# Kernel tuning notes

Measured on AMD Instinct MI355X. Metric: run time of the kernel, lower is better.

Reference implementation:

```python
import jax, jax.numpy as jnp
import numpy as np

N = 65536        # total nodes (32 graphs x 2048 nodes)
E = 1048576      # total edges (avg degree 16)
D = 64           # in_dim
H = 64           # hidden_dim
O = 32           # out_dim
B = 32           # number of graphs in the batch
NPG = 2048       # nodes per graph
EPS = 1e-5
SLOPE = 0.01     # LeakyReLU negative slope


def setup_inputs() -> dict:
    key = jax.random.key(0)
    ks = jax.random.split(key, 7)
    x = jax.random.normal(ks[0], (N, D), jnp.float32)
    edge_weights = jax.random.uniform(ks[1], (E,), jnp.float32)
    src = jax.random.randint(ks[2], (E,), 0, N, dtype=jnp.int32)
    dst = jax.random.randint(ks[3], (E,), 0, N, dtype=jnp.int32)
    graph_ids = (jnp.arange(N, dtype=jnp.int32) // NPG).astype(jnp.int32)
    # DGL GraphConv weight is (in_feats, out_feats); Linear weight is (out, in)
    W1 = jax.random.normal(ks[4], (D, H), jnp.float32) * np.float32(1.0 / np.sqrt(D))
    W2 = jax.random.normal(ks[5], (H, H), jnp.float32) * np.float32(1.0 / np.sqrt(H))
    Wc = jax.random.normal(ks[6], (O, H), jnp.float32) * np.float32(1.0 / np.sqrt(H))
    gn1_w = jnp.ones((H,), jnp.float32); gn1_b = jnp.zeros((H,), jnp.float32); gn1_a = jnp.ones((H,), jnp.float32)
    gn2_w = jnp.ones((H,), jnp.float32); gn2_b = jnp.zeros((H,), jnp.float32); gn2_a = jnp.ones((H,), jnp.float32)
    return dict(x=x, edge_weights=edge_weights, W1=W1, W2=W2, Wc=Wc,
                gn1_w=gn1_w, gn1_b=gn1_b, gn1_a=gn1_a,
                gn2_w=gn2_w, gn2_b=gn2_b, gn2_a=gn2_a,
                src=src, dst=dst, graph_ids=graph_ids)


def _graph_conv(h, W, src, dst, ew, inv_sqrt_out, inv_sqrt_in):
    # DGL GraphConv norm='both' with edge_weight:
    # out = D_in^{-1/2} * scatter_sum( ew * (D_out^{-1/2} h W)[src] -> dst )
    h = (h * inv_sqrt_out[:, None]) @ W                       # [N,H]
    m = h[src] * ew[:, None]                                  # [E,H] gather + edge weight
    agg = jax.ops.segment_sum(m, dst, num_segments=N)         # [N,H] scatter
    return agg * inv_sqrt_in[:, None]


def _graph_norm(x, w, b, a):
    # GraphNorm: (x - a*mean) / sqrt(var(x - a*mean) + eps) * w + b, stats over node dim
    mean = jnp.mean(x, axis=0, keepdims=True)
    sub = x - a * mean
    std = jnp.sqrt(jnp.mean(sub * sub, axis=0, keepdims=True) + EPS)
    return w * (sub / std) + b


def _leaky(x):
    return jnp.where(x >= 0, x, SLOPE * x)


def reference(x, edge_weights, W1, W2, Wc,
              gn1_w, gn1_b, gn1_a, gn2_w, gn2_b, gn2_a,
              src, dst, graph_ids):
    ones_e = jnp.ones((E,), x.dtype)
    deg_out = jnp.maximum(jax.ops.segment_sum(ones_e, src, num_segments=N), 1.0)
    deg_in = jnp.maximum(jax.ops.segment_sum(ones_e, dst, num_segments=N), 1.0)
    inv_so = jax.lax.rsqrt(deg_out)
    inv_si = jax.lax.rsqrt(deg_in)

    h = _graph_conv(x, W1, src, dst, edge_weights, inv_so, inv_si)
    h = _graph_norm(_leaky(h), gn1_w, gn1_b, gn1_a)
    h = _graph_conv(h, W2, src, dst, edge_weights, inv_so, inv_si)
    h = _graph_norm(_leaky(h), gn2_w, gn2_b, gn2_a)

    # dgl.mean_nodes: per-graph mean pooling
    counts = jax.ops.segment_sum(jnp.ones((N,), x.dtype), graph_ids, num_segments=B)
    pooled = jax.ops.segment_sum(h, graph_ids, num_segments=B) / counts[:, None]  # [B,H]
    return pooled @ Wc.T  # [B,O]
```

## Files before the change

kernel.cpp:

```cpp
#include <hip/hip_runtime.h>

#define N_NODES 65536
#define N_EDGES 1048576
#define B_GRAPHS 32
#define NPG     2048
#define EPS_GN  1e-5f
#define SLOPE   0.01f
#define NBUCKET 256
#define STRIDE_B 4608
#define ECAP    1024

typedef unsigned short ushort_t;
typedef unsigned int uint_t;

static __device__ __forceinline__ ushort_t f2bf(float f) {
    uint_t u = __float_as_uint(f);
    return (ushort_t)((u + 0x7FFFu + ((u >> 16) & 1u)) >> 16);
}

static __device__ __forceinline__ void acc_bf8(float4& a0, float4& a1, uint4 u, float w) {
    a0.x += __uint_as_float(u.x << 16) * w;
    a0.y += __uint_as_float(u.x & 0xffff0000u) * w;
    a0.z += __uint_as_float(u.y << 16) * w;
    a0.w += __uint_as_float(u.y & 0xffff0000u) * w;
    a1.x += __uint_as_float(u.z << 16) * w;
    a1.y += __uint_as_float(u.z & 0xffff0000u) * w;
    a1.z += __uint_as_float(u.w << 16) * w;
    a1.w += __uint_as_float(u.w & 0xffff0000u) * w;
}

__global__ __launch_bounds__(256) void hist_kernel(const int4* __restrict__ src4,
                                                   unsigned int* __restrict__ partial,
                                                   int* __restrict__ cursor) {
    __shared__ unsigned int bins[16384];
    int tid = threadIdx.x, c = blockIdx.x;
#pragma unroll
    for (int k = 0; k < 64; ++k) bins[k * 256 + tid] = 0u;
    if (c == 0) cursor[tid] = tid * STRIDE_B;
    __syncthreads();
#pragma unroll
    for (int k = 0; k < 8; ++k) {
        int4 v = src4[c * 2048 + k * 256 + tid];
        atomicAdd(&bins[v.x >> 2], 1u << ((v.x & 3) * 8));
        atomicAdd(&bins[v.y >> 2], 1u << ((v.y & 3) * 8));
        atomicAdd(&bins[v.z >> 2], 1u << ((v.z & 3) * 8));
        atomicAdd(&bins[v.w >> 2], 1u << ((v.w & 3) * 8));
    }
    __syncthreads();
    unsigned int* dstp = partial + c * 16384;
#pragma unroll
    for (int k = 0; k < 64; ++k) dstp[k * 256 + tid] = bins[k * 256 + tid];
}

__global__ __launch_bounds__(256) void reduce_src(const unsigned int* __restrict__ partial,
                                                  float4* __restrict__ inv_so4) {
    int w = blockIdx.x * 256 + threadIdx.x;
    unsigned int s0 = 0, s1 = 0, s2 = 0, s3 = 0;
#pragma unroll
    for (int c = 0; c < 128; ++c) {
        unsigned int v = partial[c * 16384 + w];
        s0 += v & 255u; s1 += (v >> 8) & 255u; s2 += (v >> 16) & 255u; s3 += v >> 24;
    }
    float4 r;
    r.x = rsqrtf((float)max((int)s0, 1));
    r.y = rsqrtf((float)max((int)s1, 1));
    r.z = rsqrtf((float)max((int)s2, 1));
    r.w = rsqrtf((float)max((int)s3, 1));
    inv_so4[w] = r;
}

__global__ __launch_bounds__(256) void bucket_scatter(const int4* __restrict__ src4,
                                                      const int4* __restrict__ dst4,
                                                      const float4* __restrict__ ew4,
                                                      int* __restrict__ cursor,
                                                      int2* __restrict__ bedges) {
    __shared__ int lhist[NBUCKET];
    __shared__ int lstart[NBUCKET];
    __shared__ int gbase[NBUCKET];
    __shared__ int sc[NBUCKET];
    __shared__ int2 staged[2048];
    int tid = threadIdx.x;
    int vbase = blockIdx.x * 512;
    lhist[tid] = 0;
    __syncthreads();
    int w0[8]; int wbr[8]; float wwt[8];
#pragma unroll
    for (int k = 0; k < 2; ++k) {
        int4 s = src4[vbase + k * 256 + tid];
        int4 d = dst4[vbase + k * 256 + tid];
        float4 w = ew4[vbase + k * 256 + tid];
        int ss[4] = {s.x, s.y, s.z, s.w};
        int dd[4] = {d.x, d.y, d.z, d.w};
        float wf[4] = {w.x, w.y, w.z, w.w};
#pragma unroll
        for (int j = 0; j < 4; ++j) {
            int b = dd[j] >> 8;
            w0[k * 4 + j] = ss[j] | ((dd[j] & 255) << 16);
            wwt[k * 4 + j] = wf[j];
            int r = atomicAdd(&lhist[b], 1);
            wbr[k * 4 + j] = (b << 16) | r;
        }
    }
    __syncthreads();
    int cnt = lhist[tid];
    sc[tid] = cnt;
    __syncthreads();
    for (int off = 1; off < 256; off <<= 1) {
        int t = (tid >= off) ? sc[tid - off] : 0;
        __syncthreads();
        sc[tid] += t;
        __syncthreads();
    }
    lstart[tid] = sc[tid] - cnt;
    gbase[tid] = cnt ? atomicAdd(&cursor[tid], cnt) : 0;
    __syncthreads();
#pragma unroll
    for (int k = 0; k < 8; ++k)
        staged[lstart[wbr[k] >> 16] + (wbr[k] & 0xFFFF)] =
            make_int2(w0[k], __float_as_int(wwt[k]));
    __syncthreads();
    int gb = gbase[tid], ls = lstart[tid];
    for (int i = 0; i < cnt; ++i)
        bedges[gb + i] = staged[ls + i];
}

__global__ __launch_bounds__(1024) void refine_kernel(const int2* __restrict__ bedges,
                                                      const int* __restrict__ cursor,
                                                      int* __restrict__ rowp,
                                                      int* __restrict__ deg,
                                                      float* __restrict__ inv_si,
                                                      int2* __restrict__ csr) {
    __shared__ int hist[4096];
    __shared__ int sc[256];
    __shared__ int2 staged[STRIDE_B];
    int tid = threadIdx.x, b = blockIdx.x;
    int e0 = b * STRIDE_B;
    int nE = cursor[b] - e0;
    for (int k = tid; k < 4096; k += 1024) hist[k] = 0;
    __syncthreads();
    for (int i = tid; i < nE; i += 1024) {
        int2 e = bedges[e0 + i];
        staged[i] = e;
        int key = (((e.x >> 16) & 255) << 4) | ((e.x & 0xFFFF) >> 12);
        atomicAdd(&hist[key], 1);
    }
    __syncthreads();
    int loc[16];
    int run = 0;
    if (tid < 256) {
        int base = tid << 4;
#pragma unroll
        for (int j = 0; j < 16; ++j) { loc[j] = run; run += hist[base + j]; }
        sc[tid] = run;
    }
    __syncthreads();
    for (int off = 1; off < 256; off <<= 1) {
        int t = (tid >= off && tid < 256) ? sc[tid - off] : 0;
        __syncthreads();
        if (tid < 256) sc[tid] += t;
        __syncthreads();
    }
    if (tid < 256) {
        int start = sc[tid] - run;
        rowp[b * 256 + tid] = e0 + start;
        deg[b * 256 + tid] = run;
        inv_si[b * 256 + tid] = rsqrtf((float)max(run, 1));
        int base = tid << 4;
#pragma unroll
        for (int j = 0; j < 16; ++j) hist[base + j] = start + loc[j];
    }
    __syncthreads();
    for (int i = tid; i < nE; i += 1024) {
        int2 e = staged[i];
        int key = (((e.x >> 16) & 255) << 4) | ((e.x & 0xFFFF) >> 12);
        int pos = atomicAdd(&hist[key], 1);
        csr[e0 + pos] = make_int2(e.x & 0xFFFF, e.y);
    }
}

__global__ __launch_bounds__(256) void gemm_f32(const float* __restrict__ in,
                                                const float* __restrict__ W,
                                                const float* __restrict__ inv_so,
                                                ushort_t* __restrict__ out_bf) {
    __shared__ float wT[64][68];
    __shared__ float xlds[16][64];
    int tid = threadIdx.x;
#pragma unroll
    for (int j = 0; j < 16; ++j) {
        int i = j * 256 + tid;
        wT[i & 63][i >> 6] = W[i];
    }
    int r0 = blockIdx.x * 16;
#pragma unroll
    for (int j = 0; j < 4; ++j) {
        int i = j * 256 + tid;
        int r = i >> 6, k = i & 63;
        int gr = r0 + r;
        xlds[r][k] = in[(size_t)gr * 64 + k] * inv_so[gr];
    }
    __syncthreads();
    int c = tid & 63;
    int rg = tid >> 6;
    float acc[4] = {0.f, 0.f, 0.f, 0.f};
#pragma unroll
    for (int k0 = 0; k0 < 64; k0 += 4) {
        float4 wv = *(const float4*)&wT[c][k0];
#pragma unroll
        for (int j = 0; j < 4; ++j) {
            float4 xv = *(const float4*)&xlds[rg * 4 + j][k0];
            acc[j] += xv.x * wv.x + xv.y * wv.y + xv.z * wv.z + xv.w * wv.w;
        }
    }
#pragma unroll
    for (int j = 0; j < 4; ++j)
        out_bf[(size_t)(r0 + rg * 4 + j) * 64 + c] = f2bf(acc[j]);
}

__global__ __launch_bounds__(256) void gemm_bf16(const ushort_t* __restrict__ in,
                                                 const float* __restrict__ W,
                                                 const float* __restrict__ inv_so,
                                                 const float* __restrict__ alpha,
                                                 const float* __restrict__ beta,
                                                 ushort_t* __restrict__ out_bf) {
    __shared__ float wT[64][68];
    __shared__ float xlds[16][64];
    int tid = threadIdx.x;
#pragma unroll
    for (int j = 0; j < 16; ++j) {
        int i = j * 256 + tid;
        wT[i & 63][i >> 6] = W[i];
    }
    int r0 = blockIdx.x * 16;
    const uint_t* inU = (const uint_t*)in;
#pragma unroll
    for (int j = 0; j < 2; ++j) {
        int idx = j * 256 + tid;
        int r = idx >> 5, kp = idx & 31;
        int gr = r0 + r;
        uint_t u = inU[(size_t)gr * 32 + kp];
        int k0 = kp * 2;
        float lo = __uint_as_float(u << 16);
        float hi = __uint_as_float(u & 0xffff0000u);
        float iso = inv_so[gr];
        xlds[r][k0]     = (alpha[k0] * lo + beta[k0]) * iso;
        xlds[r][k0 + 1] = (alpha[k0 + 1] * hi + beta[k0 + 1]) * iso;
    }
    __syncthreads();
    int c = tid & 63;
    int rg = tid >> 6;
    float acc[4] = {0.f, 0.f, 0.f, 0.f};
#pragma unroll
    for (int k0 = 0; k0 < 64; k0 += 4) {
        float4 wv = *(const float4*)&wT[c][k0];
#pragma unroll
        for (int j = 0; j < 4; ++j) {
            float4 xv = *(const float4*)&xlds[rg * 4 + j][k0];
            acc[j] += xv.x * wv.x + xv.y * wv.y + xv.z * wv.z + xv.w * wv.w;
        }
    }
#pragma unroll
    for (int j = 0; j < 4; ++j)
        out_bf[(size_t)(r0 + rg * 4 + j) * 64 + c] = f2bf(acc[j]);
}

__global__ __launch_bounds__(256) void agg_kernel(const ushort_t* __restrict__ Tb,
                                                  const int* __restrict__ rowp,
                                                  const int* __restrict__ deg,
                                                  const float* __restrict__ inv_si,
                                                  const int2* __restrict__ csr,
                                                  ushort_t* __restrict__ Yb,
                                                  float4* __restrict__ statsP4) {
    __shared__ long est[ECAP];
    int tid = threadIdx.x;
    int slot = tid >> 3;
    int node0 = blockIdx.x * 32;
    int node = node0 + slot;
    int l8 = tid & 7;
    int e_start = rowp[node0];
    int e_end = rowp[node0 + 31] + deg[node0 + 31];
    int nE = e_end - e_start;
    const long* gedge = (const long*)(csr + e_start);
    for (int i = tid; i < nE && i < ECAP; i += 256)
        est[i] = gedge[i];
    __syncthreads();
    int off = rowp[node] - e_start;
    int cnt = deg[node];
    int m1 = min(cnt, max(0, ECAP - off));
    float4 a0 = make_float4(0.f, 0.f, 0.f, 0.f);
    float4 a1 = make_float4(0.f, 0.f, 0.f, 0.f);
    int i = 0;
    for (; i + 8 <= m1; i += 8) {
        long e[8];
#pragma unroll
        for (int k = 0; k < 8; ++k) e[k] = est[off + i + k];
        uint4 t[8];
#pragma unroll
        for (int k = 0; k < 8; ++k)
            t[k] = ((const uint4*)(Tb + (((size_t)(e[k] & 0xFFFF)) << 6)))[l8];
#pragma unroll
        for (int k = 0; k < 8; ++k)
            acc_bf8(a0, a1, t[k], __int_as_float((int)(e[k] >> 32)));
    }
    for (; i < m1; ++i) {
        long e = est[off + i];
        uint4 u = ((const uint4*)(Tb + (((size_t)(e & 0xFFFF)) << 6)))[l8];
        acc_bf8(a0, a1, u, __int_as_float((int)(e >> 32)));
    }
    for (; i < cnt; ++i) {
        long e = gedge[off + i];
        uint4 u = ((const uint4*)(Tb + (((size_t)(e & 0xFFFF)) << 6)))[l8];
        acc_bf8(a0, a1, u, __int_as_float((int)(e >> 32)));
    }
    float s = inv_si[node];
    float4 v0, v1;
    v0.x = a0.x * s; v0.x = (v0.x >= 0.f) ? v0.x : SLOPE * v0.x;
    v0.y = a0.y * s; v0.y = (v0.y >= 0.f) ? v0.y : SLOPE * v0.y;
    v0.z = a0.z * s; v0.z = (v0.z >= 0.f) ? v0.z : SLOPE * v0.z;
    v0.w = a0.w * s; v0.w = (v0.w >= 0.f) ? v0.w : SLOPE * v0.w;
    v1.x = a1.x * s; v1.x = (v1.x >= 0.f) ? v1.x : SLOPE * v1.x;
    v1.y = a1.y * s; v1.y = (v1.y >= 0.f) ? v1.y : SLOPE * v1.y;
    v1.z = a1.z * s; v1.z = (v1.z >= 0.f) ? v1.z : SLOPE * v1.z;
    v1.w = a1.w * s; v1.w = (v1.w >= 0.f) ? v1.w : SLOPE * v1.w;
    if (Yb) {
        uint_t p0 = (uint_t)f2bf(v0.x) | ((uint_t)f2bf(v0.y) << 16);
        uint_t p1 = (uint_t)f2bf(v0.z) | ((uint_t)f2bf(v0.w) << 16);
        uint_t p2 = (uint_t)f2bf(v1.x) | ((uint_t)f2bf(v1.y) << 16);
        uint_t p3 = (uint_t)f2bf(v1.z) | ((uint_t)f2bf(v1.w) << 16);
        ((uint4*)Yb)[(size_t)node * 8 + l8] = make_uint4(p0, p1, p2, p3);
    }
    float4 s0 = v0, s1 = v1;
    float4 q0 = make_float4(v0.x * v0.x, v0.y * v0.y, v0.z * v0.z, v0.w * v0.w);
    float4 q1 = make_float4(v1.x * v1.x, v1.y * v1.y, v1.z * v1.z, v1.w * v1.w);
#pragma unroll
    for (int m = 8; m <= 32; m <<= 1) {
        s0.x += __shfl_xor(s0.x, m); s0.y += __shfl_xor(s0.y, m);
        s0.z += __shfl_xor(s0.z, m); s0.w += __shfl_xor(s0.w, m);
        s1.x += __shfl_xor(s1.x, m); s1.y += __shfl_xor(s1.y, m);
        s1.z += __shfl_xor(s1.z, m); s1.w += __shfl_xor(s1.w, m);
        q0.x += __shfl_xor(q0.x, m); q0.y += __shfl_xor(q0.y, m);
        q0.z += __shfl_xor(q0.z, m); q0.w += __shfl_xor(q0.w, m);
        q1.x += __shfl_xor(q1.x, m); q1.y += __shfl_xor(q1.y, m);
        q1.z += __shfl_xor(q1.z, m); q1.w += __shfl_xor(q1.w, m);
    }
    int ln = tid & 63;
    if (ln < 8) {
        float4* row = statsP4 + ((size_t)blockIdx.x * 4 + (tid >> 6)) * 32;
        row[ln * 2 + 0] = s0;
        row[ln * 2 + 1] = s1;
        row[16 + ln * 2 + 0] = q0;
        row[16 + ln * 2 + 1] = q1;
    }
}

__global__ __launch_bounds__(256) void reduce_statsA(const float* __restrict__ statsP,
                                                     float* __restrict__ slab) {
    __shared__ float red[256];
    int tid = threadIdx.x, b = blockIdx.x;
    int col = tid & 127, half = tid >> 7;
    float s = 0.f;
    for (int i = half; i < 128; i += 2)
        s += statsP[(size_t)(b * 128 + i) * 128 + col];
    red[tid] = s;
    __syncthreads();
    if (tid < 128) slab[b * 128 + tid] = red[tid] + red[tid + 128];
}

__global__ __launch_bounds__(256) void reduce_stats2(const float* __restrict__ statsP,
                                                     float* __restrict__ slab,
                                                     float* __restrict__ pooledSum) {
    __shared__ float red[256];
    int tid = threadIdx.x, b = blockIdx.x;
    if (b < 64) {
        int col = tid & 127, half = tid >> 7;
        float s = 0.f;
        for (int i = half; i < 128; i += 2)
            s += statsP[(size_t)(b * 128 + i) * 128 + col];
        red[tid] = s;
        __syncthreads();
        if (tid < 128) slab[b * 128 + tid] = red[tid] + red[tid + 128];
    } else {
        int g = b - 64;
        int col = tid & 63, part = tid >> 6;
        float s = 0.f;
        for (int r = g * 256 + part; r < (g + 1) * 256; r += 4)
            s += statsP[(size_t)r * 128 + col];
        red[tid] = s;
        __syncthreads();
        if (tid < 64)
            pooledSum[g * 64 + tid] =
                red[tid] + red[tid + 64] + red[tid + 128] + red[tid + 192];
    }
}

__global__ void finalize_kernel(const float* __restrict__ slab,
                                const float* __restrict__ w, const float* __restrict__ b,
                                const float* __restrict__ a,
                                float* __restrict__ alpha, float* __restrict__ beta) {
    int f = threadIdx.x;
    float Sy = 0.f, Qy = 0.f;
    for (int i = 0; i < 64; ++i) {
        Sy += slab[i * 128 + f];
        Qy += slab[i * 128 + 64 + f];
    }
    float m = Sy * (1.f / N_NODES);
    float q = Qy * (1.f / N_NODES);
    float af = a[f];
    float var = q - 2.f * af * m * m + af * af * m * m;
    float al = w[f] / sqrtf(var + EPS_GN);
    alpha[f] = al;
    beta[f] = b[f] - al * af * m;
}

__global__ __launch_bounds__(256) void out_kernel(const float* __restrict__ slab2,
                                                  const float* __restrict__ gn_w,
                                                  const float* __restrict__ gn_b,
                                                  const float* __restrict__ gn_a,
                                                  const float* __restrict__ pooledSum,
                                                  const float* __restrict__ Wc,
                                                  float* __restrict__ out) {
    __shared__ float al[64], be[64];
    __shared__ float p[B_GRAPHS * 64];
    int tid = threadIdx.x;
    if (tid < 64) {
        float Sy = 0.f, Qy = 0.f;
        for (int i = 0; i < 64; ++i) {
            Sy += slab2[i * 128 + tid];
            Qy += slab2[i * 128 + 64 + tid];
        }
        float m = Sy * (1.f / N_NODES);
        float q = Qy * (1.f / N_NODES);
        float af = gn_a[tid];
        float var = q - 2.f * af * m * m + af * af * m * m;
        float a_ = gn_w[tid] / sqrtf(var + EPS_GN);
        al[tid] = a_;
        be[tid] = gn_b[tid] - a_ * af * m;
    }
    __syncthreads();
    for (int i = tid; i < B_GRAPHS * 64; i += 256) {
        int f = i & 63;
        p[i] = al[f] * (pooledSum[i] * (1.f / NPG)) + be[f];
    }
    __syncthreads();
    for (int idx = tid; idx < B_GRAPHS * 32; idx += 256) {
        int g = idx >> 5, o = idx & 31;
        float acc = 0.f;
        for (int f = 0; f < 64; ++f)
            acc += p[g * 64 + f] * Wc[o * 64 + f];
        out[idx] = acc;
    }
}

extern "C" void kernel_launch(void* const* d_in, const int* in_sizes, int n_in,
                              void* d_out, int out_size, void* d_ws, size_t ws_size,
                              hipStream_t stream) {
    const float* x     = (const float*)d_in[0];
    const float* ew    = (const float*)d_in[1];
    const float* W1    = (const float*)d_in[2];
    const float* W2    = (const float*)d_in[3];
    const float* Wc    = (const float*)d_in[4];
    const float* gn1_w = (const float*)d_in[5];
    const float* gn1_b = (const float*)d_in[6];
    const float* gn1_a = (const float*)d_in[7];
    const float* gn2_w = (const float*)d_in[8];
    const float* gn2_b = (const float*)d_in[9];
    const float* gn2_a = (const float*)d_in[10];
    const int* src     = (const int*)d_in[11];
    const int* dst     = (const int*)d_in[12];

    char* ws = (char*)d_ws;
    int*   cursor    = (int*)(ws + 0);
    float* ab1       = (float*)(ws + 4096);
    float* pooledSum = (float*)(ws + 8192);
    float* slab1     = (float*)(ws + 16384);
    float* slab2     = (float*)(ws + 49152);
    int*   rowp      = (int*)(ws + 131072);
    int*   deg       = (int*)(ws + 393216);
    float* inv_so    = (float*)(ws + 655360);
    float* inv_si    = (float*)(ws + 917504);
    unsigned int* partial = (unsigned int*)(ws + (2u << 20));
    int2*  bedges    = (int2*)(ws + (10u << 20));
    int2*  csr       = (int2*)(ws + (20u << 20));
    ushort_t* Tbf    = (ushort_t*)(ws + (30u << 20));
    ushort_t* Ybf    = (ushort_t*)(ws + (38u << 20));
    float* statsP    = (float*)(ws + (46u << 20));

    hist_kernel<<<128, 256, 0, stream>>>((const int4*)src, partial, cursor);
    reduce_src<<<64, 256, 0, stream>>>(partial, (float4*)inv_so);
    bucket_scatter<<<512, 256, 0, stream>>>((const int4*)src, (const int4*)dst,
                                            (const float4*)ew, cursor, bedges);
    refine_kernel<<<NBUCKET, 1024, 0, stream>>>(bedges, cursor, rowp, deg, inv_si, csr);

    gemm_f32<<<N_NODES / 16, 256, 0, stream>>>(x, W1, inv_so, Tbf);
    agg_kernel<<<N_NODES / 32, 256, 0, stream>>>(Tbf, rowp, deg, inv_si, csr,
                                                 Ybf, (float4*)statsP);
    reduce_statsA<<<64, 256, 0, stream>>>(statsP, slab1);
    finalize_kernel<<<1, 64, 0, stream>>>(slab1, gn1_w, gn1_b, gn1_a, ab1 + 0, ab1 + 64);

    gemm_bf16<<<N_NODES / 16, 256, 0, stream>>>(Ybf, W2, inv_so, ab1 + 0, ab1 + 64, Tbf);
    agg_kernel<<<N_NODES / 32, 256, 0, stream>>>(Tbf, rowp, deg, inv_si, csr,
                                                 nullptr, (float4*)statsP);
    reduce_stats2<<<96, 256, 0, stream>>>(statsP, slab2, pooledSum);

    out_kernel<<<1, 256, 0, stream>>>(slab2, gn2_w, gn2_b, gn2_a, pooledSum, Wc,
                                      (float*)d_out);
}
```

Measured before the change: 172.5 us.

## Fuse per-bucket CSR refine into aggregation kernel, drop global CSR arrays

Removes the separate refine kernel and global CSR/rowp/deg/inv_si arrays. Each 1024-thread aggregation block now loads its bucket of 256 destination nodes, counting-sorts the edges by node in shared memory, and aggregates directly from the sorted LDS copy, computing the in-degree normalization inline. The sort is redone in both aggregation passes, adding work, but it saves a kernel launch and a global write and read of the CSR. The histogram kernel also uses half as many blocks, each covering twice the edges. Stats rows stay laid out so the existing reductions still line up, with 32 rows per 256-node block.

New measurement: 165.9 us. -3.8%, faster.

```diff
diff --git a/kernel.cpp b/kernel.cpp
--- a/kernel.cpp
+++ b/kernel.cpp
@@ -8,7 +8,6 @@
 #define SLOPE   0.01f
 #define NBUCKET 256
 #define STRIDE_B 4608
-#define ECAP    1024
 
 typedef unsigned short ushort_t;
 typedef unsigned int uint_t;
@@ -39,8 +38,8 @@
     if (c == 0) cursor[tid] = tid * STRIDE_B;
     __syncthreads();
 #pragma unroll
-    for (int k = 0; k < 8; ++k) {
-        int4 v = src4[c * 2048 + k * 256 + tid];
+    for (int k = 0; k < 16; ++k) {
+        int4 v = src4[c * 4096 + k * 256 + tid];
         atomicAdd(&bins[v.x >> 2], 1u << ((v.x & 3) * 8));
         atomicAdd(&bins[v.y >> 2], 1u << ((v.y & 3) * 8));
         atomicAdd(&bins[v.z >> 2], 1u << ((v.z & 3) * 8));
@@ -57,7 +56,7 @@
     int w = blockIdx.x * 256 + threadIdx.x;
     unsigned int s0 = 0, s1 = 0, s2 = 0, s3 = 0;
 #pragma unroll
-    for (int c = 0; c < 128; ++c) {
+    for (int c = 0; c < 64; ++c) {
         unsigned int v = partial[c * 16384 + w];
         s0 += v & 255u; s1 += (v >> 8) & 255u; s2 += (v >> 16) & 255u; s3 += v >> 24;
     }
@@ -124,60 +123,6 @@
         bedges[gb + i] = staged[ls + i];
 }
 
-__global__ __launch_bounds__(1024) void refine_kernel(const int2* __restrict__ bedges,
-                                                      const int* __restrict__ cursor,
-                                                      int* __restrict__ rowp,
-                                                      int* __restrict__ deg,
-                                                      float* __restrict__ inv_si,
-                                                      int2* __restrict__ csr) {
-    __shared__ int hist[4096];
-    __shared__ int sc[256];
-    __shared__ int2 staged[STRIDE_B];
-    int tid = threadIdx.x, b = blockIdx.x;
-    int e0 = b * STRIDE_B;
-    int nE = cursor[b] - e0;
-    for (int k = tid; k < 4096; k += 1024) hist[k] = 0;
-    __syncthreads();
-    for (int i = tid; i < nE; i += 1024) {
-        int2 e = bedges[e0 + i];
-        staged[i] = e;
-        int key = (((e.x >> 16) & 255) << 4) | ((e.x & 0xFFFF) >> 12);
-        atomicAdd(&hist[key], 1);
-    }
-    __syncthreads();
-    int loc[16];
-    int run = 0;
-    if (tid < 256) {
-        int base = tid << 4;
-#pragma unroll
-        for (int j = 0; j < 16; ++j) { loc[j] = run; run += hist[base + j]; }
-        sc[tid] = run;
-    }
-    __syncthreads();
-    for (int off = 1; off < 256; off <<= 1) {
-        int t = (tid >= off && tid < 256) ? sc[tid - off] : 0;
-        __syncthreads();
-        if (tid < 256) sc[tid] += t;
-        __syncthreads();
-    }
-    if (tid < 256) {
-        int start = sc[tid] - run;
-        rowp[b * 256 + tid] = e0 + start;
-        deg[b * 256 + tid] = run;
-        inv_si[b * 256 + tid] = rsqrtf((float)max(run, 1));
-        int base = tid << 4;
-#pragma unroll
-        for (int j = 0; j < 16; ++j) hist[base + j] = start + loc[j];
-    }
-    __syncthreads();
-    for (int i = tid; i < nE; i += 1024) {
-        int2 e = staged[i];
-        int key = (((e.x >> 16) & 255) << 4) | ((e.x & 0xFFFF) >> 12);
-        int pos = atomicAdd(&hist[key], 1);
-        csr[e0 + pos] = make_int2(e.x & 0xFFFF, e.y);
-    }
-}
-
 __global__ __launch_bounds__(256) void gemm_f32(const float* __restrict__ in,
                                                 const float* __restrict__ W,
                                                 const float* __restrict__ inv_so,
@@ -263,92 +208,118 @@
         out_bf[(size_t)(r0 + rg * 4 + j) * 64 + c] = f2bf(acc[j]);
 }
 
-__global__ __launch_bounds__(256) void agg_kernel(const ushort_t* __restrict__ Tb,
-                                                  const int* __restrict__ rowp,
-                                                  const int* __restrict__ deg,
-                                                  const float* __restrict__ inv_si,
-                                                  const int2* __restrict__ csr,
+__global__ __launch_bounds__(1024) void agg_fused(const ushort_t* __restrict__ Tb,
+                                                  const int2* __restrict__ bedges,
+                                                  const int* __restrict__ cursor,
                                                   ushort_t* __restrict__ Yb,
                                                   float4* __restrict__ statsP4) {
-    __shared__ long est[ECAP];
-    int tid = threadIdx.x;
-    int slot = tid >> 3;
-    int node0 = blockIdx.x * 32;
-    int node = node0 + slot;
+    __shared__ int2 staged[STRIDE_B];
+    __shared__ int2 sorted[STRIDE_B];
+    __shared__ int hist[256];
+    __shared__ int sc[256];
+    __shared__ int nstart[256];
+    __shared__ int ndeg[256];
+    int tid = threadIdx.x, b = blockIdx.x;
+    int e0 = b * STRIDE_B;
+    int nE = cursor[b] - e0;
+    if (tid < 256) hist[tid] = 0;
+    __syncthreads();
+    for (int i = tid; i < nE; i += 1024) {
+        int2 e = bedges[e0 + i];
+        staged[i] = e;
+        atomicAdd(&hist[(e.x >> 16) & 255], 1);
+    }
+    __syncthreads();
+    if (tid < 256) sc[tid] = hist[tid];
+    __syncthreads();
+    for (int off = 1; off < 256; off <<= 1) {
+        int t = (tid >= off && tid < 256) ? sc[tid - off] : 0;
+        __syncthreads();
+        if (tid < 256) sc[tid] += t;
+        __syncthreads();
+    }
+    if (tid < 256) {
+        int cnt = hist[tid];
+        int start = sc[tid] - cnt;
+        nstart[tid] = start;
+        ndeg[tid] = cnt;
+        hist[tid] = start;
+    }
+    __syncthreads();
+    for (int i = tid; i < nE; i += 1024) {
+        int2 e = staged[i];
+        int pos = atomicAdd(&hist[(e.x >> 16) & 255], 1);
+        sorted[pos] = make_int2(e.x & 0xFFFF, e.y);
+    }
+    __syncthreads();
+    const long* sl = (const long*)sorted;
     int l8 = tid & 7;
-    int e_start = rowp[node0];
-    int e_end = rowp[node0 + 31] + deg[node0 + 31];
-    int nE = e_end - e_start;
-    const long* gedge = (const long*)(csr + e_start);
-    for (int i = tid; i < nE && i < ECAP; i += 256)
-        est[i] = gedge[i];
-    __syncthreads();
-    int off = rowp[node] - e_start;
-    int cnt = deg[node];
-    int m1 = min(cnt, max(0, ECAP - off));
-    float4 a0 = make_float4(0.f, 0.f, 0.f, 0.f);
-    float4 a1 = make_float4(0.f, 0.f, 0.f, 0.f);
-    int i = 0;
-    for (; i + 8 <= m1; i += 8) {
-        long e[8];
-#pragma unroll
-        for (int k = 0; k < 8; ++k) e[k] = est[off + i + k];
-        uint4 t[8];
-#pragma unroll
-        for (int k = 0; k < 8; ++k)
-            t[k] = ((const uint4*)(Tb + (((size_t)(e[k] & 0xFFFF)) << 6)))[l8];
-#pragma unroll
-        for (int k = 0; k < 8; ++k)
-            acc_bf8(a0, a1, t[k], __int_as_float((int)(e[k] >> 32)));
-    }
-    for (; i < m1; ++i) {
-        long e = est[off + i];
-        uint4 u = ((const uint4*)(Tb + (((size_t)(e & 0xFFFF)) << 6)))[l8];
-        acc_bf8(a0, a1, u, __int_as_float((int)(e >> 32)));
-    }
-    for (; i < cnt; ++i) {
-        long e = gedge[off + i];
-        uint4 u = ((const uint4*)(Tb + (((size_t)(e & 0xFFFF)) << 6)))[l8];
-        acc_bf8(a0, a1, u, __int_as_float((int)(e >> 32)));
-    }
-    float s = inv_si[node];
-    float4 v0, v1;
-    v0.x = a0.x * s; v0.x = (v0.x >= 0.f) ? v0.x : SLOPE * v0.x;
-    v0.y = a0.y * s; v0.y = (v0.y >= 0.f) ? v0.y : SLOPE * v0.y;
-    v0.z = a0.z * s; v0.z = (v0.z >= 0.f) ? v0.z : SLOPE * v0.z;
-    v0.w = a0.w * s; v0.w = (v0.w >= 0.f) ? v0.w : SLOPE * v0.w;
-    v1.x = a1.x * s; v1.x = (v1.x >= 0.f) ? v1.x : SLOPE * v1.x;
-    v1.y = a1.y * s; v1.y = (v1.y >= 0.f) ? v1.y : SLOPE * v1.y;
-    v1.z = a1.z * s; v1.z = (v1.z >= 0.f) ? v1.z : SLOPE * v1.z;
-    v1.w = a1.w * s; v1.w = (v1.w >= 0.f) ? v1.w : SLOPE * v1.w;
-    if (Yb) {
-        uint_t p0 = (uint_t)f2bf(v0.x) | ((uint_t)f2bf(v0.y) << 16);
-        uint_t p1 = (uint_t)f2bf(v0.z) | ((uint_t)f2bf(v0.w) << 16);
-        uint_t p2 = (uint_t)f2bf(v1.x) | ((uint_t)f2bf(v1.y) << 16);
-        uint_t p3 = (uint_t)f2bf(v1.z) | ((uint_t)f2bf(v1.w) << 16);
-        ((uint4*)Yb)[(size_t)node * 8 + l8] = make_uint4(p0, p1, p2, p3);
-    }
-    float4 s0 = v0, s1 = v1;
-    float4 q0 = make_float4(v0.x * v0.x, v0.y * v0.y, v0.z * v0.z, v0.w * v0.w);
-    float4 q1 = make_float4(v1.x * v1.x, v1.y * v1.y, v1.z * v1.z, v1.w * v1.w);
-#pragma unroll
-    for (int m = 8; m <= 32; m <<= 1) {
-        s0.x += __shfl_xor(s0.x, m); s0.y += __shfl_xor(s0.y, m);
-        s0.z += __shfl_xor(s0.z, m); s0.w += __shfl_xor(s0.w, m);
-        s1.x += __shfl_xor(s1.x, m); s1.y += __shfl_xor(s1.y, m);
-        s1.z += __shfl_xor(s1.z, m); s1.w += __shfl_xor(s1.w, m);
-        q0.x += __shfl_xor(q0.x, m); q0.y += __shfl_xor(q0.y, m);
-        q0.z += __shfl_xor(q0.z, m); q0.w += __shfl_xor(q0.w, m);
-        q1.x += __shfl_xor(q1.x, m); q1.y += __shfl_xor(q1.y, m);
-        q1.z += __shfl_xor(q1.z, m); q1.w += __shfl_xor(q1.w, m);
-    }
+    int wv = tid >> 6;
     int ln = tid & 63;
-    if (ln < 8) {
-        float4* row = statsP4 + ((size_t)blockIdx.x * 4 + (tid >> 6)) * 32;
-        row[ln * 2 + 0] = s0;
-        row[ln * 2 + 1] = s1;
-        row[16 + ln * 2 + 0] = q0;
-        row[16 + ln * 2 + 1] = q1;
+#pragma unroll
+    for (int pass = 0; pass < 2; ++pass) {
+        int nl = pass * 128 + (tid >> 3);
+        int node = b * 256 + nl;
+        int off = nstart[nl];
+        int cnt = ndeg[nl];
+        float4 a0 = make_float4(0.f, 0.f, 0.f, 0.f);
+        float4 a1 = make_float4(0.f, 0.f, 0.f, 0.f);
+        int i = 0;
+        for (; i + 8 <= cnt; i += 8) {
+            long e[8];
+#pragma unroll
+            for (int k = 0; k < 8; ++k) e[k] = sl[off + i + k];
+            uint4 t[8];
+#pragma unroll
+            for (int k = 0; k < 8; ++k)
+                t[k] = ((const uint4*)(Tb + (((size_t)(e[k] & 0xFFFF)) << 6)))[l8];
+#pragma unroll
+            for (int k = 0; k < 8; ++k)
+                acc_bf8(a0, a1, t[k], __int_as_float((int)(e[k] >> 32)));
+        }
+        for (; i < cnt; ++i) {
+            long e = sl[off + i];
+            uint4 u = ((const uint4*)(Tb + (((size_t)(e & 0xFFFF)) << 6)))[l8];
+            acc_bf8(a0, a1, u, __int_as_float((int)(e >> 32)));
+        }
+        float s = rsqrtf((float)max(cnt, 1));
+        float4 v0, v1;
+        v0.x = a0.x * s; v0.x = (v0.x >= 0.f) ? v0.x : SLOPE * v0.x;
+        v0.y = a0.y * s; v0.y = (v0.y >= 0.f) ? v0.y : SLOPE * v0.y;
+        v0.z = a0.z * s; v0.z = (v0.z >= 0.f) ? v0.z : SLOPE * v0.z;
+        v0.w = a0.w * s; v0.w = (v0.w >= 0.f) ? v0.w : SLOPE * v0.w;
+        v1.x = a1.x * s; v1.x = (v1.x >= 0.f) ? v1.x : SLOPE * v1.x;
+        v1.y = a1.y * s; v1.y = (v1.y >= 0.f) ? v1.y : SLOPE * v1.y;
+        v1.z = a1.z * s; v1.z = (v1.z >= 0.f) ? v1.z : SLOPE * v1.z;
+        v1.w = a1.w * s; v1.w = (v1.w >= 0.f) ? v1.w : SLOPE * v1.w;
+        if (Yb) {
+            uint_t p0 = (uint_t)f2bf(v0.x) | ((uint_t)f2bf(v0.y) << 16);
+            uint_t p1 = (uint_t)f2bf(v0.z) | ((uint_t)f2bf(v0.w) << 16);
+            uint_t p2 = (uint_t)f2bf(v1.x) | ((uint_t)f2bf(v1.y) << 16);
+            uint_t p3 = (uint_t)f2bf(v1.z) | ((uint_t)f2bf(v1.w) << 16);
+            ((uint4*)Yb)[(size_t)node * 8 + l8] = make_uint4(p0, p1, p2, p3);
+        }
+        float4 s0 = v0, s1 = v1;
+        float4 q0 = make_float4(v0.x * v0.x, v0.y * v0.y, v0.z * v0.z, v0.w * v0.w);
+        float4 q1 = make_float4(v1.x * v1.x, v1.y * v1.y, v1.z * v1.z, v1.w * v1.w);
+#pragma unroll
+        for (int m = 8; m <= 32; m <<= 1) {
+            s0.x += __shfl_xor(s0.x, m); s0.y += __shfl_xor(s0.y, m);
+            s0.z += __shfl_xor(s0.z, m); s0.w += __shfl_xor(s0.w, m);
+            s1.x += __shfl_xor(s1.x, m); s1.y += __shfl_xor(s1.y, m);
+            s1.z += __shfl_xor(s1.z, m); s1.w += __shfl_xor(s1.w, m);
+            q0.x += __shfl_xor(q0.x, m); q0.y += __shfl_xor(q0.y, m);
+            q0.z += __shfl_xor(q0.z, m); q0.w += __shfl_xor(q0.w, m);
+            q1.x += __shfl_xor(q1.x, m); q1.y += __shfl_xor(q1.y, m);
+            q1.z += __shfl_xor(q1.z, m); q1.w += __shfl_xor(q1.w, m);
+        }
+        if (ln < 8) {
+            float4* row = statsP4 + ((size_t)b * 32 + pass * 16 + wv) * 32;
+            row[ln * 2 + 0] = s0;
+            row[ln * 2 + 1] = s1;
+            row[16 + ln * 2 + 0] = q0;
+            row[16 + ln * 2 + 1] = q1;
+        }
     }
 }
 
@@ -473,32 +444,25 @@
     float* pooledSum = (float*)(ws + 8192);
     float* slab1     = (float*)(ws + 16384);
     float* slab2     = (float*)(ws + 49152);
-    int*   rowp      = (int*)(ws + 131072);
-    int*   deg       = (int*)(ws + 393216);
     float* inv_so    = (float*)(ws + 655360);
-    float* inv_si    = (float*)(ws + 917504);
     unsigned int* partial = (unsigned int*)(ws + (2u << 20));
     int2*  bedges    = (int2*)(ws + (10u << 20));
-    int2*  csr       = (int2*)(ws + (20u << 20));
-    ushort_t* Tbf    = (ushort_t*)(ws + (30u << 20));
-    ushort_t* Ybf    = (ushort_t*)(ws + (38u << 20));
-    float* statsP    = (float*)(ws + (46u << 20));
-
-    hist_kernel<<<128, 256, 0, stream>>>((const int4*)src, partial, cursor);
+    ushort_t* Tbf    = (ushort_t*)(ws + (20u << 20));
+    ushort_t* Ybf    = (ushort_t*)(ws + (28u << 20));
+    float* statsP    = (float*)(ws + (36u << 20));
+
+    hist_kernel<<<64, 256, 0, stream>>>((const int4*)src, partial, cursor);
     reduce_src<<<64, 256, 0, stream>>>(partial, (float4*)inv_so);
     bucket_scatter<<<512, 256, 0, stream>>>((const int4*)src, (const int4*)dst,
                                             (const float4*)ew, cursor, bedges);
-    refine_kernel<<<NBUCKET, 1024, 0, stream>>>(bedges, cursor, rowp, deg, inv_si, csr);
 
     gemm_f32<<<N_NODES / 16, 256, 0, stream>>>(x, W1, inv_so, Tbf);
-    agg_kernel<<<N_NODES / 32, 256, 0, stream>>>(Tbf, rowp, deg, inv_si, csr,
-                                                 Ybf, (float4*)statsP);
+    agg_fused<<<NBUCKET, 1024, 0, stream>>>(Tbf, bedges, cursor, Ybf, (float4*)statsP);
     reduce_statsA<<<64, 256, 0, stream>>>(statsP, slab1);
     finalize_kernel<<<1, 64, 0, stream>>>(slab1, gn1_w, gn1_b, gn1_a, ab1 + 0, ab1 + 64);
 
     gemm_bf16<<<N_NODES / 16, 256, 0, stream>>>(Ybf, W2, inv_so, ab1 + 0, ab1 + 64, Tbf);
-    agg_kernel<<<N_NODES / 32, 256, 0, stream>>>(Tbf, rowp, deg, inv_si, csr,
-                                                 nullptr, (float4*)statsP);
+    agg_fused<<<NBUCKET, 1024, 0, stream>>>(Tbf, bedges, cursor, nullptr, (float4*)statsP);
     reduce_stats2<<<96, 256, 0, stream>>>(statsP, slab2, pooledSum);
 
     out_kernel<<<1, 256, 0, stream>>>(slab2, gn2_w, gn2_b, gn2_a, pooledSum, Wc,
```
